# Optimization experiments

Hardware: AMD Instinct MI355X
Metric: run time of the kernel (lower is better)

The kernel has to match this reference:

```python
import jax, jax.numpy as jnp
import numpy as np

ACT_DIM = 768
DICT_SIZE = 32768
S0 = 4096          # top-level latent size (dict_size // prod(lower sizes))
S1 = 8             # lower_level_latent_sizes[0]
K = 64             # per-token top-k (applied globally as k * batch)


def setup_inputs() -> dict:
    key = jax.random.key(0)
    ks = jax.random.split(key, 7)
    scale_e = 1.0 / np.sqrt(ACT_DIM)
    scale_d = 1.0 / np.sqrt(DICT_SIZE)
    return {
        "x": jax.random.normal(ks[0], (4096, ACT_DIM), dtype=jnp.float32),
        "W0": jax.random.normal(ks[1], (S0, ACT_DIM), dtype=jnp.float32) * scale_e,
        "b0": jnp.zeros((S0,), dtype=jnp.float32),
        "W1": jax.random.normal(ks[2], (DICT_SIZE, ACT_DIM), dtype=jnp.float32) * scale_e,
        "b1": jnp.zeros((DICT_SIZE,), dtype=jnp.float32),
        "Wd": jax.random.normal(ks[3], (ACT_DIM, DICT_SIZE), dtype=jnp.float32) * scale_d,
        "b_dec": jnp.zeros((ACT_DIM,), dtype=jnp.float32),
    }


def reference(x, W0, b0, W1, b1, Wd, b_dec):
    B = x.shape[0]
    x_centered = x - b_dec                                   # [B, D]
    # hierarchical relu encoders
    l0 = jax.nn.relu(x_centered @ W0.T + b0)                 # [B, S0]
    l1 = jax.nn.relu(x_centered @ W1.T + b1)                 # [B, S0*S1]
    # multiplicative gating: lower-level gate broadcast over finest level
    final_dense = (l1.reshape(B, S0, S1) * l0[:, :, None]).reshape(B, S0 * S1)
    # global batch top-k over flattened [B * dict_size]
    flat = final_dense.reshape(-1)
    k_for_batch = min(K * B, flat.shape[0])
    vals, idx = jax.lax.top_k(flat, k_for_batch)
    sparse_flat = jnp.zeros_like(flat).at[idx].set(vals)
    encoded = sparse_flat.reshape(B, S0 * S1)
    # decode
    x_hat = encoded @ Wd.T + b_dec                           # [B, D]
    return x_hat
```

## Files before the change

### kernel.cpp

```cpp
#include <hip/hip_runtime.h>
#include <stdint.h>

#define DDIM 768
#define BROWS 4096
#define S0N 4096
#define DICT 32768
#define KTOT 262144u
#define PREF 2.0f
#define DELTA 4e-3f
#define CAND_CAP 8388608u
#define BAND_CAP 4096

static constexpr size_t OFF_XH   = 0;
static constexpr size_t OFF_XL   = 6291456;
static constexpr size_t OFF_W0H  = 12582912;
static constexpr size_t OFF_W0L  = 18874368;
static constexpr size_t OFF_W1H  = 25165824;
static constexpr size_t OFF_W1L  = 75497472;
static constexpr size_t OFF_WDT  = 0;
static constexpr size_t OFF_L0   = 125829120;
static constexpr size_t OFF_CTRL = 192937984;
static constexpr size_t OFF_ROWC = 193069056;
static constexpr size_t OFF_ROWD = 193085440;
static constexpr size_t OFF_CAND = 201474048;
static constexpr size_t WS_NEED  = 268582912;


typedef __attribute__((ext_vector_type(8))) short bf16x8;
typedef __attribute__((ext_vector_type(4))) float f32x4;

__device__ __forceinline__ unsigned umin_(unsigned a, unsigned b) { return a < b ? a : b; }
__device__ __forceinline__ float relu_(float v) { return v > 0.f ? v : 0.f; }

__device__ __forceinline__ unsigned short f2bf(float f) {
    union { float f; unsigned u; } v; v.f = f;
    unsigned r = v.u + 0x7FFFu + ((v.u >> 16) & 1u);
    return (unsigned short)(r >> 16);
}
__device__ __forceinline__ float bf2f(unsigned short h) {
    union { float f; unsigned u; } v; v.u = ((unsigned)h) << 16;
    return v.f;
}
__device__ __forceinline__ void split1(float a, short& h, short& l) {
    unsigned short hb = f2bf(a);
    float rem = a - bf2f(hb);
    h = (short)hb;
    l = (short)f2bf(rem);
}

__device__ __forceinline__ void gl16(const void* g, void* l) {
    __builtin_amdgcn_global_load_lds(
        (const __attribute__((address_space(1))) void*)g,
        (__attribute__((address_space(3))) void*)l,
        16, 0, 0);
}

__global__ void k_split_x(const float* __restrict__ x, const float* __restrict__ b_dec,
                          short* __restrict__ XH, short* __restrict__ XL) {
    int i = blockIdx.x * 256 + threadIdx.x;
    float4 xv = ((const float4*)x)[i];
    int d = (i % (DDIM / 4)) * 4;
    float4 bv = *(const float4*)(b_dec + d);
    float a[4] = {xv.x - bv.x, xv.y - bv.y, xv.z - bv.z, xv.w - bv.w};
    short4 h, lo;
    split1(a[0], h.x, lo.x); split1(a[1], h.y, lo.y);
    split1(a[2], h.z, lo.z); split1(a[3], h.w, lo.w);
    ((short4*)XH)[i] = h;
    ((short4*)XL)[i] = lo;
}

__global__ void k_split_w(const float* __restrict__ W, short* __restrict__ H,
                          short* __restrict__ L) {
    int i = blockIdx.x * 256 + threadIdx.x;
    float4 wv = ((const float4*)W)[i];
    short4 h, lo;
    split1(wv.x, h.x, lo.x); split1(wv.y, h.y, lo.y);
    split1(wv.z, h.z, lo.z); split1(wv.w, h.w, lo.w);
    ((short4*)H)[i] = h;
    ((short4*)L)[i] = lo;
}

__global__ void k_transpose(const float* __restrict__ Wd, float* __restrict__ WdT) {
    __shared__ float tile[32][33];
    int j0 = blockIdx.x * 32, d0 = blockIdx.y * 32;
    int tx = threadIdx.x & 31, ty = threadIdx.x >> 5;
#pragma unroll
    for (int i = 0; i < 4; ++i)
        tile[ty + i * 8][tx] = Wd[(size_t)(d0 + ty + i * 8) * DICT + j0 + tx];
    __syncthreads();
#pragma unroll
    for (int i = 0; i < 4; ++i)
        WdT[(size_t)(j0 + ty + i * 8) * DDIM + d0 + tx] = tile[tx][ty + i * 8];
}

template<int EPI>
__launch_bounds__(512, 2) __global__
void k_mm(const short* __restrict__ XH, const short* __restrict__ XL,
          const short* __restrict__ WH, const short* __restrict__ WL,
          const float* __restrict__ bias, float* __restrict__ l0buf,
          uint2* __restrict__ cand, unsigned* __restrict__ ctrl) {
    __shared__ __align__(16) char smem[131072];

    const int t = threadIdx.x;
    const int w = t >> 6, l = t & 63;
    const int wm = w >> 2, wn = w & 3;
    const int lr = l & 15, lk = l >> 4;

    const int nwg = gridDim.x;
    const int bid = blockIdx.x;
    const int swz = (bid & 7) * (nwg >> 3) + (bid >> 3);
    const int bm = (swz & 15) << 8;
    const int bn = (swz >> 4) << 8;

    unsigned idxA[4], idxB[4];
#pragma unroll
    for (int q = 0; q < 4; ++q) {
        const int ab = w * 4 + q;
        idxA[q] = (unsigned)(bm + (ab >> 4) * 128 + ((ab >> 1) & 7) * 16 + lr) * 768u
                + (unsigned)((ab & 1) * 32 + lk * 8);
        idxB[q] = (unsigned)(bn + (ab >> 3) * 64 + ((ab >> 1) & 3) * 16 + lr) * 768u
                + (unsigned)((ab & 1) * 32 + lk * 8);
    }

    f32x4 acc[8][4];
#pragma unroll
    for (int i = 0; i < 8; ++i)
#pragma unroll
        for (int j = 0; j < 4; ++j) acc[i][j] = (f32x4){0.f, 0.f, 0.f, 0.f};

#pragma unroll
    for (int q = 0; q < 4; ++q) {
        gl16(XH + idxA[q], smem + (w * 4 + q) * 1024);
        gl16(WH + idxB[q], smem + 65536 + (w * 4 + q) * 1024);
    }

    for (int kt = 0; kt < 36; ++kt) {
        const int cur = kt & 1;
        __builtin_amdgcn_s_barrier();
        const int ktn = kt + 1;
        if (ktn < 36) {
            const short* An; const short* Bn; unsigned kbn;
            if (ktn < 12)      { An = XH; Bn = WH; kbn = (unsigned)ktn * 64u; }
            else if (ktn < 24) { An = XH; Bn = WL; kbn = (unsigned)(ktn - 12) * 64u; }
            else               { An = XL; Bn = WH; kbn = (unsigned)(ktn - 24) * 64u; }
            char* stA = smem + (cur ^ 1) * 32768;
            char* stB = smem + 65536 + (cur ^ 1) * 32768;
#pragma unroll
            for (int q = 0; q < 4; ++q) {
                gl16(An + idxA[q] + kbn, stA + (w * 4 + q) * 1024);
                gl16(Bn + idxB[q] + kbn, stB + (w * 4 + q) * 1024);
            }
            asm volatile("s_waitcnt vmcnt(8)" ::: "memory");
        } else {
            asm volatile("s_waitcnt vmcnt(0)" ::: "memory");
        }
        __builtin_amdgcn_s_barrier();

        const short* rA = (const short*)(smem + cur * 32768);
        const short* rB = (const short*)(smem + 65536 + cur * 32768);
        __builtin_amdgcn_s_setprio(1);
#pragma unroll
        for (int ks = 0; ks < 2; ++ks) {
            bf16x8 bfr[4];
#pragma unroll
            for (int nj = 0; nj < 4; ++nj)
                bfr[nj] = *(const bf16x8*)(rB + ((wn * 8 + nj * 2 + ks) * 1024 + l * 16) / 2);
#pragma unroll
            for (int mi = 0; mi < 8; ++mi) {
                bf16x8 af = *(const bf16x8*)(rA + ((wm * 16 + mi * 2 + ks) * 1024 + l * 16) / 2);
#pragma unroll
                for (int nj = 0; nj < 4; ++nj)
                    acc[mi][nj] = __builtin_amdgcn_mfma_f32_16x16x32_bf16(
                        af, bfr[nj], acc[mi][nj], 0, 0, 0);
            }
        }
        __builtin_amdgcn_s_setprio(0);
    }
    __syncthreads();

    if constexpr (EPI == 0) {
#pragma unroll
        for (int mi = 0; mi < 8; ++mi) {
#pragma unroll
            for (int r = 0; r < 4; ++r) {
                const int row = bm + wm * 128 + mi * 16 + lk * 4 + r;
                float* orow = l0buf + (size_t)row * S0N;
#pragma unroll
                for (int nj = 0; nj < 4; ++nj) {
                    const int col = bn + wn * 64 + nj * 16 + lr;
                    orow[col] = relu_(acc[mi][nj][r] + bias[col]);
                }
            }
        }
    } else {
        unsigned* pscan = (unsigned*)smem;
        unsigned cnt = 0;
#pragma unroll
        for (int mi = 0; mi < 8; ++mi)
#pragma unroll
            for (int nj = 0; nj < 4; ++nj)
#pragma unroll
                for (int r = 0; r < 4; ++r) {
                    const int row = bm + wm * 128 + mi * 16 + lk * 4 + r;
                    const int col = bn + wn * 64 + nj * 16 + lr;
                    float v = relu_(acc[mi][nj][r] + bias[col]);
                    v *= l0buf[(size_t)row * S0N + (col >> 3)];
                    acc[mi][nj][r] = v;
                    cnt += (v >= PREF) ? 1u : 0u;
                }
        pscan[t] = cnt;
        __syncthreads();
        for (int s = 1; s < 512; s <<= 1) {
            unsigned v2 = (t >= s) ? pscan[t - s] : 0u;
            __syncthreads();
            pscan[t] += v2;
            __syncthreads();
        }
        if (t == 511) pscan[512] = atomicAdd(&ctrl[0], pscan[511]);
        __syncthreads();
        unsigned off = pscan[512] + pscan[t] - cnt;
#pragma unroll
        for (int mi = 0; mi < 8; ++mi)
#pragma unroll
            for (int nj = 0; nj < 4; ++nj)
#pragma unroll
                for (int r = 0; r < 4; ++r) {
                    const float v = acc[mi][nj][r];
                    if (v >= PREF) {
                        const int row = bm + wm * 128 + mi * 16 + lk * 4 + r;
                        const int col = bn + wn * 64 + nj * 16 + lr;
                        if (off < CAND_CAP)
                            cand[off] = make_uint2(__float_as_uint(v),
                                                   ((unsigned)row << 15) | (unsigned)col);
                        ++off;
                    }
                }
    }
}

__global__ void k_hist1(const uint2* __restrict__ cand, unsigned* __restrict__ ctrl) {
    __shared__ unsigned h[2048];
    for (int i = threadIdx.x; i < 2048; i += 256) h[i] = 0;
    __syncthreads();
    unsigned n = umin_(ctrl[0], CAND_CAP);
    for (unsigned i = blockIdx.x * 256 + threadIdx.x; i < n; i += gridDim.x * 256)
        atomicAdd(&h[cand[i].x >> 20], 1u);
    __syncthreads();
    unsigned* hist = ctrl + 256;
    for (int i = threadIdx.x; i < 2048; i += 256)
        if (h[i]) atomicAdd(&hist[i], h[i]);
}

__global__ void k_scan1(unsigned* __restrict__ ctrl) {
    __shared__ unsigned hs[2048];
    __shared__ unsigned cs[256];
    const unsigned* h = ctrl + 256;
    int t = threadIdx.x;
    for (int i = t; i < 2048; i += 256) hs[i] = h[i];
    __syncthreads();
    unsigned s = 0;
    for (int b = 0; b < 8; ++b) s += hs[t * 8 + b];
    cs[t] = s;
    __syncthreads();
    if (t == 0) {
        unsigned cum = 0, T = 0, cb = 0;
        for (int c = 255; c >= 0; --c) {
            if (cum + cs[c] >= KTOT) {
                for (int b = c * 8 + 7; b >= c * 8; --b) {
                    cum += hs[b];
                    if (cum >= KTOT) { T = (unsigned)b; cb = cum - hs[b]; break; }
                }
                break;
            }
            cum += cs[c];
        }
        ctrl[1] = T; ctrl[2] = cb;
    }
}

__global__ void k_hist2(const uint2* __restrict__ cand, unsigned* __restrict__ ctrl) {
    unsigned n = umin_(ctrl[0], CAND_CAP);
    unsigned T = ctrl[1];
    unsigned* hist2 = ctrl + 2304;
    for (unsigned i = blockIdx.x * 256 + threadIdx.x; i < n; i += gridDim.x * 256) {
        unsigned u = cand[i].x;
        if ((u >> 20) == T) atomicAdd(&hist2[(u >> 8) & 0xFFFu], 1u);
    }
}

__global__ void k_scan2(unsigned* __restrict__ ctrl) {
    __shared__ unsigned hs[4096];
    __shared__ unsigned cs[256];
    const unsigned* h = ctrl + 2304;
    int t = threadIdx.x;
    for (int i = t; i < 4096; i += 256) hs[i] = h[i];
    __syncthreads();
    unsigned s = 0;
    for (int b = 0; b < 16; ++b) s += hs[t * 16 + b];
    cs[t] = s;
    __syncthreads();
    if (t == 0) {
        unsigned cum = ctrl[2], T2 = 0;
        for (int c = 255; c >= 0; --c) {
            if (cum + cs[c] >= KTOT) {
                for (int b = c * 16 + 15; b >= c * 16; --b) {
                    cum += hs[b];
                    if (cum >= KTOT) { T2 = (unsigned)b; break; }
                }
                break;
            }
            cum += cs[c];
        }
        ctrl[3] = (ctrl[1] << 12) | T2;
    }
}

__global__ void k_band(const uint2* __restrict__ cand, unsigned* __restrict__ ctrl) {
    __shared__ unsigned lhi;
    if (threadIdx.x == 0) lhi = 0;
    __syncthreads();
    unsigned n = umin_(ctrl[0], CAND_CAP);
    unsigned H = ctrl[3];
    float lo = __uint_as_float(H << 8) - DELTA;
    float hi = __uint_as_float((H + 1u) << 8) + DELTA;
    unsigned* band_idx = ctrl + 6400;
    unsigned my = 0;
    for (unsigned i = blockIdx.x * 256 + threadIdx.x; i < n; i += gridDim.x * 256) {
        float v = __uint_as_float(cand[i].x);
        if (v > hi) ++my;
        else if (v >= lo) {
            unsigned p = atomicAdd(&ctrl[5], 1u);
            if (p < BAND_CAP) band_idx[p] = cand[i].y;
        }
    }
    atomicAdd(&lhi, my);
    __syncthreads();
    if (threadIdx.x == 0 && lhi) atomicAdd(&ctrl[4], lhi);
}

__global__ void k_f64(const float* __restrict__ x, const float* __restrict__ b_dec,
                      const float* __restrict__ W0, const float* __restrict__ b0,
                      const float* __restrict__ W1, const float* __restrict__ b1,
                      const unsigned* __restrict__ ctrl, double* __restrict__ band_v) {
    unsigned n = umin_(ctrl[5], BAND_CAP);
    unsigned bi = blockIdx.x;
    if (bi >= n) return;
    const unsigned* band_idx = ctrl + 6400;
    unsigned idx = band_idx[bi];
    int b = idx >> 15, j = idx & 32767, s0 = j >> 3;
    int lane = threadIdx.x;
    const float* xr = x + (size_t)b * DDIM;
    const float* w1 = W1 + (size_t)j * DDIM;
    const float* w0 = W0 + (size_t)s0 * DDIM;
    double d1 = 0.0, d0 = 0.0;
    for (int k = lane; k < DDIM; k += 64) {
        double xv = (double)xr[k] - (double)b_dec[k];
        d1 += xv * (double)w1[k];
        d0 += xv * (double)w0[k];
    }
    for (int off = 32; off; off >>= 1) {
        d1 += __shfl_down(d1, off);
        d0 += __shfl_down(d0, off);
    }
    if (lane == 0) {
        double l1v = d1 + (double)b1[j];  l1v = l1v > 0.0 ? l1v : 0.0;
        double l0v = d0 + (double)b0[s0]; l0v = l0v > 0.0 ? l0v : 0.0;
        band_v[bi] = l1v * l0v;
    }
}

__global__ void k_final(unsigned* __restrict__ ctrl, const double* __restrict__ band_v,
                        uint2* __restrict__ extra) {
    __shared__ unsigned long long skey[BAND_CAP];
    __shared__ unsigned sidx[BAND_CAP];
    int t = threadIdx.x;
    unsigned n = umin_(ctrl[5], BAND_CAP);
    const unsigned* band_idx = ctrl + 6400;
    for (int i = t; i < BAND_CAP; i += 256) {
        if ((unsigned)i < n) {
            skey[i] = (unsigned long long)__double_as_longlong(band_v[i]);
            sidx[i] = band_idx[i];
        } else {
            skey[i] = 0ull; sidx[i] = 0xFFFFFFFFu;
        }
    }
    __syncthreads();
    for (int kk = 2; kk <= BAND_CAP; kk <<= 1) {
        for (int jj = kk >> 1; jj > 0; jj >>= 1) {
            for (int i = t; i < BAND_CAP; i += 256) {
                int ixj = i ^ jj;
                if (ixj > i) {
                    unsigned long long ka = skey[i], kb = skey[ixj];
                    unsigned ia = sidx[i], ib = sidx[ixj];
                    bool ab = (ka > kb) || (ka == kb && ia < ib);
                    bool asc = ((i & kk) == 0);
                    if (asc ? !ab : ab) {
                        skey[i] = kb; skey[ixj] = ka;
                        sidx[i] = ib; sidx[ixj] = ia;
                    }
                }
            }
            __syncthreads();
        }
    }
    unsigned c_hi = ctrl[4];
    unsigned k_rem = (c_hi < KTOT) ? (KTOT - c_hi) : 0u;
    if (k_rem > n) k_rem = n;
    if (t == 0) ctrl[6] = k_rem;
    for (unsigned i = t; i < k_rem; i += 256)
        extra[i] = make_uint2(sidx[i],
                              __float_as_uint((float)__longlong_as_double((long long)skey[i])));
}

__global__ void k_rows_a(const uint2* __restrict__ cand, const unsigned* __restrict__ ctrl,
                         unsigned* __restrict__ rowc, uint2* __restrict__ rowd) {
    unsigned n = umin_(ctrl[0], CAND_CAP);
    unsigned H = ctrl[3];
    float hi = __uint_as_float((H + 1u) << 8) + DELTA;
    for (unsigned i = blockIdx.x * 256 + threadIdx.x; i < n; i += gridDim.x * 256) {
        unsigned u = cand[i].x;
        if (__uint_as_float(u) > hi) {
            unsigned idx = cand[i].y;
            unsigned b = idx >> 15;
            unsigned p = atomicAdd(&rowc[b], 1u);
            if (p < 256u) rowd[(b << 8) + p] = make_uint2(idx & 32767u, u);
        }
    }
}

__global__ void k_rows_b(const unsigned* __restrict__ ctrl, const uint2* __restrict__ extra,
                         unsigned* __restrict__ rowc, uint2* __restrict__ rowd) {
    unsigned k_rem = ctrl[6];
    for (unsigned i = blockIdx.x * 256 + threadIdx.x; i < k_rem; i += gridDim.x * 256) {
        unsigned idx = extra[i].x;
        unsigned b = idx >> 15;
        unsigned p = atomicAdd(&rowc[b], 1u);
        if (p < 256u) rowd[(b << 8) + p] = make_uint2(idx & 32767u, extra[i].y);
    }
}

__launch_bounds__(256) __global__
void k_decode(const uint2* __restrict__ rowd, const unsigned* __restrict__ rowc,
              const float* __restrict__ WdT, const float* __restrict__ b_dec,
              float* __restrict__ out) {
    __shared__ uint2 e[256];
    int b = blockIdx.x, t = threadIdx.x;
    unsigned c = rowc[b]; if (c > 256u) c = 256u;
    if ((unsigned)t < c) e[t] = rowd[(b << 8) + t];
    __syncthreads();
    float a0 = b_dec[t], a1 = b_dec[t + 256], a2 = b_dec[t + 512];
#pragma unroll 4
    for (unsigned i = 0; i < c; ++i) {
        float v = __uint_as_float(e[i].y);
        const float* w = WdT + (size_t)e[i].x * DDIM;
        a0 = fmaf(v, w[t], a0);
        a1 = fmaf(v, w[t + 256], a1);
        a2 = fmaf(v, w[t + 512], a2);
    }
    float* o = out + (size_t)b * DDIM;
    o[t] = a0; o[t + 256] = a1; o[t + 512] = a2;
}

extern "C" void kernel_launch(void* const* d_in, const int* in_sizes, int n_in,
                              void* d_out, int out_size, void* d_ws, size_t ws_size,
                              hipStream_t stream) {
    const float* x     = (const float*)d_in[0];
    const float* W0    = (const float*)d_in[1];
    const float* b0    = (const float*)d_in[2];
    const float* W1    = (const float*)d_in[3];
    const float* b1    = (const float*)d_in[4];
    const float* Wd    = (const float*)d_in[5];
    const float* b_dec = (const float*)d_in[6];
    float* out = (float*)d_out;

    if (ws_size < WS_NEED) {
        hipMemsetAsync(d_out, 0, (size_t)out_size * sizeof(float), stream);
        return;
    }

    char* ws = (char*)d_ws;
    short*    XH     = (short*)(ws + OFF_XH);
    short*    XL     = (short*)(ws + OFF_XL);
    short*    W0H    = (short*)(ws + OFF_W0H);
    short*    W0L    = (short*)(ws + OFF_W0L);
    short*    W1H    = (short*)(ws + OFF_W1H);
    short*    W1L    = (short*)(ws + OFF_W1L);
    float*    WdT    = (float*)(ws + OFF_WDT);
    float*    l0     = (float*)(ws + OFF_L0);
    unsigned* ctrl   = (unsigned*)(ws + OFF_CTRL);
    double*   band_v = (double*)(ws + OFF_CTRL + 65536);
    uint2*    extra  = (uint2*)(ws + OFF_CTRL + 98304);
    unsigned* rowc   = (unsigned*)(ws + OFF_ROWC);
    uint2*    rowd   = (uint2*)(ws + OFF_ROWD);
    uint2*    cand   = (uint2*)(ws + OFF_CAND);

    hipMemsetAsync(ctrl, 0, 6400 * sizeof(unsigned), stream);
    hipMemsetAsync(rowc, 0, BROWS * sizeof(unsigned), stream);

    k_split_x<<<(BROWS * DDIM / 4) / 256, 256, 0, stream>>>(x, b_dec, XH, XL);
    k_split_w<<<(S0N * DDIM / 4) / 256, 256, 0, stream>>>(W0, W0H, W0L);
    k_split_w<<<(DICT * DDIM / 4) / 256, 256, 0, stream>>>(W1, W1H, W1L);

    k_mm<0><<<(S0N / 256) * 16, 512, 0, stream>>>(XH, XL, W0H, W0L, b0, l0, nullptr, nullptr);
    k_mm<1><<<(DICT / 256) * 16, 512, 0, stream>>>(XH, XL, W1H, W1L, b1, l0, cand, ctrl);

    k_transpose<<<dim3(DICT / 32, DDIM / 32), 256, 0, stream>>>(Wd, WdT);

    k_hist1<<<1024, 256, 0, stream>>>(cand, ctrl);
    k_scan1<<<1, 256, 0, stream>>>(ctrl);
    k_hist2<<<1024, 256, 0, stream>>>(cand, ctrl);
    k_scan2<<<1, 256, 0, stream>>>(ctrl);
    k_band<<<1024, 256, 0, stream>>>(cand, ctrl);
    k_f64<<<BAND_CAP, 64, 0, stream>>>(x, b_dec, W0, b0, W1, b1, ctrl, band_v);
    k_final<<<1, 256, 0, stream>>>(ctrl, band_v, extra);

    k_rows_a<<<1024, 256, 0, stream>>>(cand, ctrl, rowc, rowd);
    k_rows_b<<<32, 256, 0, stream>>>(ctrl, extra, rowc, rowd);
    k_decode<<<BROWS, 256, 0, stream>>>(rowd, rowc, WdT, b_dec, out);
}
```

Baseline: 1.368 ms.

## Deepen GEMM pipeline to four half-K LDS stages with interleaved loads

The bf16 split-precision GEMM main loop changes from double-buffered 64-wide K tiles with two barriers per step to a four-slot ring of 32-wide K half-tiles. Loads run three stages ahead, and each step needs only one barrier. Global-to-LDS loads for A and B are split and placed between the two MFMA halves, so memory traffic overlaps compute and synchronisation stalls shrink. In exchange, the loop has twice as many iterations and fragment register pressure changes, with a tighter dependence on hand-tuned vmcnt waits.

Result: faster. 1.207 ms (-11.8%).

```diff
diff --git a/kernel.cpp b/kernel.cpp
--- a/kernel.cpp
+++ b/kernel.cpp
@@ -112,15 +112,11 @@
     const int bm = (swz & 15) << 8;
     const int bn = (swz >> 4) << 8;
 
-    unsigned idxA[4], idxB[4];
-#pragma unroll
-    for (int q = 0; q < 4; ++q) {
-        const int ab = w * 4 + q;
-        idxA[q] = (unsigned)(bm + (ab >> 4) * 128 + ((ab >> 1) & 7) * 16 + lr) * 768u
-                + (unsigned)((ab & 1) * 32 + lk * 8);
-        idxB[q] = (unsigned)(bn + (ab >> 3) * 64 + ((ab >> 1) & 3) * 16 + lr) * 768u
-                + (unsigned)((ab & 1) * 32 + lk * 8);
-    }
+    const int a0 = 2 * w, a1 = a0 + 1;
+    const unsigned aB0 = (unsigned)(bm + (a0 >> 3) * 128 + (a0 & 7) * 16 + lr) * 768u + (unsigned)(lk * 8);
+    const unsigned aB1 = (unsigned)(bm + (a1 >> 3) * 128 + (a1 & 7) * 16 + lr) * 768u + (unsigned)(lk * 8);
+    const unsigned bB0 = (unsigned)(bn + (a0 >> 2) * 64 + (a0 & 3) * 16 + lr) * 768u + (unsigned)(lk * 8);
+    const unsigned bB1 = (unsigned)(bn + (a1 >> 2) * 64 + (a1 & 3) * 16 + lr) * 768u + (unsigned)(lk * 8);
 
     f32x4 acc[8][4];
 #pragma unroll
@@ -129,51 +125,68 @@
         for (int j = 0; j < 4; ++j) acc[i][j] = (f32x4){0.f, 0.f, 0.f, 0.f};
 
 #pragma unroll
-    for (int q = 0; q < 4; ++q) {
-        gl16(XH + idxA[q], smem + (w * 4 + q) * 1024);
-        gl16(WH + idxB[q], smem + 65536 + (w * 4 + q) * 1024);
-    }
-
-    for (int kt = 0; kt < 36; ++kt) {
-        const int cur = kt & 1;
+    for (int J = 0; J < 3; ++J) {
+        const unsigned kb = (unsigned)J * 32u;
+        char* dA = smem + J * 16384 + a0 * 1024;
+        char* dB = smem + 65536 + J * 16384 + a0 * 1024;
+        gl16(XH + aB0 + kb, dA);
+        gl16(XH + aB1 + kb, dA + 1024);
+        gl16(WH + bB0 + kb, dB);
+        gl16(WH + bB1 + kb, dB + 1024);
+    }
+
+#pragma unroll 1
+    for (int H = 0; H < 72; ++H) {
+        if (H < 70)       asm volatile("s_waitcnt vmcnt(8)" ::: "memory");
+        else if (H == 70) asm volatile("s_waitcnt vmcnt(4)" ::: "memory");
+        else              asm volatile("s_waitcnt vmcnt(0)" ::: "memory");
         __builtin_amdgcn_s_barrier();
-        const int ktn = kt + 1;
-        if (ktn < 36) {
-            const short* An; const short* Bn; unsigned kbn;
-            if (ktn < 12)      { An = XH; Bn = WH; kbn = (unsigned)ktn * 64u; }
-            else if (ktn < 24) { An = XH; Bn = WL; kbn = (unsigned)(ktn - 12) * 64u; }
-            else               { An = XL; Bn = WH; kbn = (unsigned)(ktn - 24) * 64u; }
-            char* stA = smem + (cur ^ 1) * 32768;
-            char* stB = smem + 65536 + (cur ^ 1) * 32768;
-#pragma unroll
-            for (int q = 0; q < 4; ++q) {
-                gl16(An + idxA[q] + kbn, stA + (w * 4 + q) * 1024);
-                gl16(Bn + idxB[q] + kbn, stB + (w * 4 + q) * 1024);
-            }
-            asm volatile("s_waitcnt vmcnt(8)" ::: "memory");
-        } else {
-            asm volatile("s_waitcnt vmcnt(0)" ::: "memory");
-        }
-        __builtin_amdgcn_s_barrier();
-
-        const short* rA = (const short*)(smem + cur * 32768);
-        const short* rB = (const short*)(smem + 65536 + cur * 32768);
+
+        const char* rA = smem + (H & 3) * 16384;
+        const char* rB = smem + 65536 + (H & 3) * 16384;
+
+        const int J = H + 3;
+        const short* As = XH; const short* Bs = WH; unsigned kb = 0;
+        char* dA = nullptr; char* dB = nullptr;
+        const bool hj = J < 72;
+        if (hj) {
+            const int ktJ = J >> 1;
+            if (ktJ < 12)      { As = XH; Bs = WH; kb = (unsigned)ktJ * 64u; }
+            else if (ktJ < 24) { As = XH; Bs = WL; kb = (unsigned)(ktJ - 12) * 64u; }
+            else               { As = XL; Bs = WH; kb = (unsigned)(ktJ - 24) * 64u; }
+            kb += (unsigned)(J & 1) * 32u;
+            dA = smem + (J & 3) * 16384 + a0 * 1024;
+            dB = smem + 65536 + (J & 3) * 16384 + a0 * 1024;
+        }
+
+        bf16x8 bfr[4], af[4];
+#pragma unroll
+        for (int nj = 0; nj < 4; ++nj)
+            bfr[nj] = *(const bf16x8*)(rB + (wn * 4 + nj) * 1024 + l * 16);
+#pragma unroll
+        for (int m2 = 0; m2 < 4; ++m2)
+            af[m2] = *(const bf16x8*)(rA + (wm * 8 + m2) * 1024 + l * 16);
+        if (hj) { gl16(As + aB0 + kb, dA); gl16(As + aB1 + kb, dA + 1024); }
         __builtin_amdgcn_s_setprio(1);
 #pragma unroll
-        for (int ks = 0; ks < 2; ++ks) {
-            bf16x8 bfr[4];
+        for (int m2 = 0; m2 < 4; ++m2)
 #pragma unroll
             for (int nj = 0; nj < 4; ++nj)
-                bfr[nj] = *(const bf16x8*)(rB + ((wn * 8 + nj * 2 + ks) * 1024 + l * 16) / 2);
-#pragma unroll
-            for (int mi = 0; mi < 8; ++mi) {
-                bf16x8 af = *(const bf16x8*)(rA + ((wm * 16 + mi * 2 + ks) * 1024 + l * 16) / 2);
-#pragma unroll
-                for (int nj = 0; nj < 4; ++nj)
-                    acc[mi][nj] = __builtin_amdgcn_mfma_f32_16x16x32_bf16(
-                        af, bfr[nj], acc[mi][nj], 0, 0, 0);
-            }
-        }
+                acc[m2][nj] = __builtin_amdgcn_mfma_f32_16x16x32_bf16(
+                    af[m2], bfr[nj], acc[m2][nj], 0, 0, 0);
+        __builtin_amdgcn_s_setprio(0);
+
+#pragma unroll
+        for (int m2 = 0; m2 < 4; ++m2)
+            af[m2] = *(const bf16x8*)(rA + (wm * 8 + 4 + m2) * 1024 + l * 16);
+        if (hj) { gl16(Bs + bB0 + kb, dB); gl16(Bs + bB1 + kb, dB + 1024); }
+        __builtin_amdgcn_s_setprio(1);
+#pragma unroll
+        for (int m2 = 0; m2 < 4; ++m2)
+#pragma unroll
+            for (int nj = 0; nj < 4; ++nj)
+                acc[4 + m2][nj] = __builtin_amdgcn_mfma_f32_16x16x32_bf16(
+                    af[m2], bfr[nj], acc[4 + m2][nj], 0, 0, 0);
         __builtin_amdgcn_s_setprio(0);
     }
     __syncthreads();
```
